# Kernel optimization log

Hardware: AMD Instinct MI355X
Metric: run time of the kernel (lower is better)

## Reference

```python
import itertools
import jax, jax.numpy as jnp
import numpy as np


def _lin(x, w, b):
    # LogitsInference with logic_hidden_dim=[] is a single Linear (logits).
    return jnp.einsum('...i,oi->...o', x, w) + b


def _permute_cat(x, order):
    # Permutation(order): concat over all permutations of the `order` variable axes.
    if order <= 1:
        return x
    nd = x.ndim  # [B, n x order, C]
    return jnp.concatenate(
        [jnp.transpose(x, (0,) + p + (nd - 1,))
         for p in itertools.permutations(range(1, order + 1))], axis=-1)


def _expand(x, i, n):
    # Expander(i-1): insert a new object axis at position i (after existing var axes).
    x = jnp.expand_dims(x, axis=i)
    shape = list(x.shape)
    shape[i] = n
    return jnp.broadcast_to(x, tuple(shape))


def _reduce(x, order_in):
    # Reducer(order_in, exclude_self=True): mask entries with repeated indices among
    # the order_in variable axes, then take exists(max)/forall(min) over the last
    # variable axis and interleave channels -> 2*C.
    n = x.shape[1]
    if order_in >= 2:
        idx = [jnp.arange(n).reshape((1,) * k + (n,) + (1,) * (order_in - k - 1))
               for k in range(order_in)]
        mask = jnp.ones((n,) * order_in, dtype=bool)
        for a in range(order_in):
            for b in range(a + 1, order_in):
                mask = mask & (idx[a] != idx[b])
        mask = mask[None, ..., None]  # [1, n x order_in, 1]
        inp0 = jnp.where(mask, x, jnp.zeros((), x.dtype))
        inp1 = jnp.where(mask, x, jnp.ones((), x.dtype))
    else:
        inp0 = inp1 = x
    exists = jnp.max(inp0, axis=-2)
    forall = jnp.min(inp1, axis=-2)
    out = jnp.stack([exists, forall], axis=-1)  # interleave like torch stack+view
    return out.reshape(out.shape[:-2] + (out.shape[-2] * 2,))


def _bmask(act, bit, ndim):
    return act[:, bit].astype(jnp.float32).reshape((-1,) + (1,) * (ndim - 1))


def _logic_layer(x0, x1, x2, x3,
                 w_op0, b_op0, w_red0, b_red0,
                 w_exp1, b_exp1, w_op1, b_op1, w_red1, b_red1,
                 w_exp2, b_exp2, w_op2, b_op2, w_red2, b_red2,
                 w_exp3, b_exp3, w_op3, b_op3, act):
    n = x1.shape[1]
    # Per-batch-item bit masks replace index_select/index_copy_ (same math:
    # selected rows get the branch output, others contribute zero to the sum).
    # order 0: bits 0 (direct), 1 (reduce from order 1)
    s0 = (_bmask(act, 0, 2) * _lin(x0, w_op0, b_op0)
          + _bmask(act, 1, 2) * _lin(_reduce(x1, 1), w_red0, b_red0))
    o0 = jnp.where(jnp.any(act[:, 0:2] == 1), jax.nn.sigmoid(s0), jnp.zeros_like(s0))
    # order 1: bits 2 (expand from 0), 3 (direct), 4 (reduce from 2)
    s1 = (_bmask(act, 2, 3) * _lin(_expand(x0, 1, n), w_exp1, b_exp1)
          + _bmask(act, 3, 3) * _lin(x1, w_op1, b_op1)
          + _bmask(act, 4, 3) * _lin(_reduce(x2, 2), w_red1, b_red1))
    o1 = jnp.where(jnp.any(act[:, 2:5] == 1), jax.nn.sigmoid(s1), jnp.zeros_like(s1))
    # order 2: bits 5 (expand), 6 (direct), 7 (reduce)
    s2 = (_bmask(act, 5, 4) * _lin(_permute_cat(_expand(x1, 2, n), 2), w_exp2, b_exp2)
          + _bmask(act, 6, 4) * _lin(_permute_cat(x2, 2), w_op2, b_op2)
          + _bmask(act, 7, 4) * _lin(_permute_cat(_reduce(x3, 3), 2), w_red2, b_red2))
    o2 = jnp.where(jnp.any(act[:, 5:8] == 1), jax.nn.sigmoid(s2), jnp.zeros_like(s2))
    # order 3 (= max_order): bits 8 (expand), 9 (direct)
    s3 = (_bmask(act, 8, 5) * _lin(_permute_cat(_expand(x2, 3, n), 3), w_exp3, b_exp3)
          + _bmask(act, 9, 5) * _lin(_permute_cat(x3, 3), w_op3, b_op3))
    o3 = jnp.where(jnp.any(act[:, 8:10] == 1), jax.nn.sigmoid(s3), jnp.zeros_like(s3))
    return (o0, o1, o2, o3)


def setup_inputs() -> dict:
    key = jax.random.key(0)
    B, n, C, O = 8, 32, 64, 64
    ks = list(jax.random.split(key, 32))
    ki = iter(ks)
    d = {}
    d['x0'] = jax.random.normal(next(ki), (B, C), jnp.float32)
    d['x1'] = jax.random.normal(next(ki), (B, n, C), jnp.float32)
    d['x2'] = jax.random.normal(next(ki), (B, n, n, C), jnp.float32)
    d['x3'] = jax.random.normal(next(ki), (B, n, n, n, C), jnp.float32)
    in_dims = {'w_op0': C, 'w_red0': 2 * C,
               'w_exp1': C, 'w_op1': C, 'w_red1': 2 * C,
               'w_exp2': 2 * C, 'w_op2': 2 * C, 'w_red2': 4 * C,
               'w_exp3': 6 * C, 'w_op3': 6 * C}
    for name, ind in in_dims.items():
        d[name] = jax.random.normal(next(ki), (O, ind), jnp.float32) * 0.05
        d['b' + name[1:]] = jnp.zeros((O,), jnp.float32)
    d['act'] = jax.random.randint(next(ki), (B, 10), 0, 2, dtype=jnp.int32)
    return d


def reference(x0, x1, x2, x3,
              w_op0, b_op0, w_red0, b_red0,
              w_exp1, b_exp1, w_op1, b_op1, w_red1, b_red1,
              w_exp2, b_exp2, w_op2, b_op2, w_red2, b_red2,
              w_exp3, b_exp3, w_op3, b_op3, act):
    return _logic_layer(x0, x1, x2, x3,
                        w_op0, b_op0, w_red0, b_red0,
                        w_exp1, b_exp1, w_op1, b_op1, w_red1, b_red1,
                        w_exp2, b_exp2, w_op2, b_op2, w_red2, b_red2,
                        w_exp3, b_exp3, w_op3, b_op3, act)
```

## Files before the change

### kernel.cpp

```cpp
#include <hip/hip_runtime.h>
#include <hip/hip_bf16.h>
#include <math.h>

#define NB 8
#define NN 32
#define NC 64
#define NO 64

#define WS_G    0
#define WS_MF   16
#define WS_R1   128
#define WS_R2   2048
#define WS_X1B  36864
#define WS_X2B  45056
#define WS_R3B  307200
#define WS_BB   831488
#define WS_BB2  832000
#define WS_WC   832512
#define WS_WC2  1029120
#define WS_R2B  1160192
#define WS_WC1  1176576
#define WS_X0B  1242112
#define WS_BB1  1242368

typedef short bf16x8 __attribute__((ext_vector_type(8)));
typedef unsigned short u16x4 __attribute__((ext_vector_type(4)));
typedef float f32x4 __attribute__((ext_vector_type(4)));

__device__ __forceinline__ float sigmoidf_(float s) {
    return 1.0f / (1.0f + expf(-s));
}

__device__ __forceinline__ unsigned short f2b(float x) {
    union { __hip_bfloat16 h; unsigned short u; } v;
    v.h = __float2bfloat16(x);
    return v.u;
}

__device__ __forceinline__ float b2f(unsigned short u) {
    union { unsigned int u; float f; } v; v.u = ((unsigned int)u) << 16;
    return v.f;
}

__global__ __launch_bounds__(256) void prep_all(
        const float* __restrict__ x0, const float* __restrict__ x1,
        const float* __restrict__ x2,
        const float* __restrict__ we3, const float* __restrict__ wo3,
        const float* __restrict__ we2, const float* __restrict__ wo2,
        const float* __restrict__ wr2,
        const float* __restrict__ we1, const float* __restrict__ wo1,
        const float* __restrict__ wr1,
        const float* __restrict__ be1, const float* __restrict__ bo1,
        const float* __restrict__ br1,
        const float* __restrict__ be2, const float* __restrict__ bo2,
        const float* __restrict__ br2,
        const float* __restrict__ be3, const float* __restrict__ bo3,
        const int* __restrict__ act, float* __restrict__ ws) {
    __shared__ float pmx[4][64], pmn[4][64];
    int bb = blockIdx.x, t = threadIdx.x;
    if (bb < 1536) {
        int tid = bb * 256 + t;
        unsigned short* wc = (unsigned short*)(ws + WS_WC);
        int i8 = tid & 7;
        int lane = (tid >> 3) & 63;
        int rest = tid >> 9;
        int kk = rest % 24;
        int ntb = rest / 24;
        int nt = ntb & 3, b = ntb >> 2;
        int o = nt * 16 + (lane & 15);
        int kloc = kk * 32 + ((lane >> 4) << 3) + i8;
        bool m8 = act[b * 10 + 8] == 1;
        bool m9 = act[b * 10 + 9] == 1;
        float val;
        if (kloc < 384) val = m8 ? we3[o * 384 + kloc] : 0.0f;
        else            val = m9 ? wo3[o * 384 + kloc - 384] : 0.0f;
        wc[tid] = f2b(val);
    } else if (bb < 2560) {
        int tid = (bb - 1536) * 256 + t;
        unsigned short* wc2 = (unsigned short*)(ws + WS_WC2);
        int i8 = tid & 7;
        int lane = (tid >> 3) & 63;
        int rest = tid >> 9;
        int kk = rest & 15;
        int ntb = rest >> 4;
        int nt = ntb & 3, b = ntb >> 2;
        int o = nt * 16 + (lane & 15);
        int kloc = kk * 32 + ((lane >> 4) << 3) + i8;
        float val;
        if (kloc < 128)      val = (act[b * 10 + 5] == 1) ? we2[o * 128 + kloc] : 0.0f;
        else if (kloc < 256) val = (act[b * 10 + 6] == 1) ? wo2[o * 128 + kloc - 128] : 0.0f;
        else                 val = (act[b * 10 + 7] == 1) ? wr2[o * 256 + kloc - 256] : 0.0f;
        wc2[tid] = f2b(val);
    } else if (bb < 3072) {
        int tid = (bb - 2560) * 256 + t;
        unsigned short* wc1 = (unsigned short*)(ws + WS_WC1);
        int i8 = tid & 7;
        int lane = (tid >> 3) & 63;
        int rest = tid >> 9;
        int kk = rest & 7;
        int ntb = rest >> 3;
        int nt = ntb & 3, b = ntb >> 2;
        int o = nt * 16 + (lane & 15);
        int kloc = kk * 32 + ((lane >> 4) << 3) + i8;
        float val;
        if (kloc < 64)       val = (act[b * 10 + 2] == 1) ? we1[o * 64 + kloc] : 0.0f;
        else if (kloc < 128) val = (act[b * 10 + 3] == 1) ? wo1[o * 64 + kloc - 64] : 0.0f;
        else                 val = (act[b * 10 + 4] == 1) ? wr1[o * 128 + kloc - 128] : 0.0f;
        wc1[tid] = f2b(val);
    } else if (bb < 3074) {
        int t512 = (bb - 3072) * 256 + t;
        int b = t512 >> 6, o = t512 & 63;
        float m2 = (act[b * 10 + 2] == 1) ? 1.0f : 0.0f;
        float m3 = (act[b * 10 + 3] == 1) ? 1.0f : 0.0f;
        float m4 = (act[b * 10 + 4] == 1) ? 1.0f : 0.0f;
        float m5 = (act[b * 10 + 5] == 1) ? 1.0f : 0.0f;
        float m6 = (act[b * 10 + 6] == 1) ? 1.0f : 0.0f;
        float m7 = (act[b * 10 + 7] == 1) ? 1.0f : 0.0f;
        float m8 = (act[b * 10 + 8] == 1) ? 1.0f : 0.0f;
        float m9 = (act[b * 10 + 9] == 1) ? 1.0f : 0.0f;
        ws[WS_BB1 + t512] = m2 * be1[o] + m3 * bo1[o] + m4 * br1[o];
        ws[WS_BB2 + t512] = m5 * be2[o] + m6 * bo2[o] + m7 * br2[o];
        ws[WS_BB  + t512] = m8 * be3[o] + m9 * bo3[o];
        unsigned short* x0b = (unsigned short*)(ws + WS_X0B);
        x0b[t512] = f2b(x0[t512]);
        if (t512 < 80) ws[WS_MF + t512] = (act[t512] == 1) ? 1.0f : 0.0f;
        if (t512 < 4) {
            const int lo[4] = {0, 2, 5, 8};
            const int hi[4] = {2, 5, 8, 10};
            int any = 0;
            for (int bx = 0; bx < NB; ++bx)
                for (int bit = lo[t512]; bit < hi[t512]; ++bit)
                    any |= (act[bx * 10 + bit] == 1);
            ws[WS_G + t512] = any ? 1.0f : 0.0f;
        }
    } else if (bb < 3082) {
        if (t < 64) {
            int b = bb - 3074, c = t;
            unsigned short* x1b = (unsigned short*)(ws + WS_X1B);
            float mx = -INFINITY, mn = INFINITY;
            for (int k = 0; k < NN; ++k) {
                float v = x1[(b * NN + k) * NC + c];
                x1b[(b * NN + k) * NC + c] = f2b(v);
                mx = fmaxf(mx, v); mn = fminf(mn, v);
            }
            ws[WS_R1 + b * 2 * NC + 2 * c]     = mx;
            ws[WS_R1 + b * 2 * NC + 2 * c + 1] = mn;
        }
    } else {
        int idx = bb - 3082;
        int i = idx & 31, b = idx >> 5;
        int w = t >> 6, c = t & 63;
        unsigned short* x2b = (unsigned short*)(ws + WS_X2B);
        float mx = -INFINITY, mn = INFINITY;
        #pragma unroll
        for (int q = 0; q < 8; ++q) {
            int jj = w * 8 + q;
            float v = x2[((b * NN + i) * NN + jj) * NC + c];
            x2b[((b * NN + i) * NN + jj) * NC + c] = f2b(v);
            mx = fmaxf(mx, (jj == i) ? 0.0f : v);
            mn = fminf(mn, (jj == i) ? 1.0f : v);
        }
        pmx[w][c] = mx; pmn[w][c] = mn;
        __syncthreads();
        if (t < 64) {
            mx = fmaxf(fmaxf(pmx[0][c], pmx[1][c]), fmaxf(pmx[2][c], pmx[3][c]));
            mn = fminf(fminf(pmn[0][c], pmn[1][c]), fminf(pmn[2][c], pmn[3][c]));
            unsigned short* r2b = (unsigned short*)(ws + WS_R2B);
            unsigned int packed = (unsigned int)f2b(mx) | ((unsigned int)f2b(mn) << 16);
            *(unsigned int*)(r2b + (b * NN + i) * 128 + 2 * c) = packed;
        }
    }
}

__global__ __launch_bounds__(256) void out3k_pair(
        const float* __restrict__ x3, const float* __restrict__ ws_f,
        float* __restrict__ out) {
    __shared__ unsigned short A[32 * 768];
    int blk = blockIdx.x;
    int b = blk / 528, pi = blk - b * 528;
    float fsq = sqrtf(4225.0f - 8.0f * (float)pi);
    int i = (int)((65.0f - fsq) * 0.5f);
    while (i > 0 && (i * (65 - i)) / 2 > pi) --i;
    while (((i + 1) * (64 - i)) / 2 <= pi) ++i;
    int j = i + (pi - (i * (65 - i)) / 2);

    int t = threadIdx.x;
    int lane = t & 63, wv = t >> 6;
    const unsigned short* x2b = (const unsigned short*)(ws_f + WS_X2B);
    const unsigned short* wc = (const unsigned short*)(ws_f + WS_WC);
    char* Ab = (char*)A;

    {
        int r8 = t >> 3, c8 = (t & 7) << 3;
        size_t cb[6]; int cs[6];
        cb[0] = ((b * 32 + i) * 32 + j) * 64; cs[0] = 0;
        cb[1] = ((b * 32 + i) * 32) * 64;     cs[1] = 64;
        cb[2] = ((b * 32 + j) * 32 + i) * 64; cs[2] = 0;
        cb[3] = (b * 1024 + i) * 64;          cs[3] = 2048;
        cb[4] = ((b * 32 + j) * 32) * 64;     cs[4] = 64;
        cb[5] = (b * 1024 + j) * 64;          cs[5] = 2048;
        int sw = (r8 & 7) << 4;
        #pragma unroll
        for (int ch = 0; ch < 6; ++ch) {
            bf16x8 v = *(const bf16x8*)(x2b + cb[ch] + (size_t)r8 * cs[ch] + c8);
            *(bf16x8*)(Ab + ((r8 * 1536 + (ch * 64 + c8) * 2) ^ sw)) = v;
        }
        int r16 = t >> 4, c4 = (t & 15) << 2;
        const float* xb[6]; int xs[6];
        xb[0] = x3 + (size_t)(((b * 32 + i) * 32 + j) * 32) * 64; xs[0] = 64;
        xb[1] = x3 + (size_t)(((b * 32 + i) * 32) * 32 + j) * 64; xs[1] = 2048;
        xb[2] = x3 + (size_t)(((b * 32 + j) * 32 + i) * 32) * 64; xs[2] = 64;
        xb[3] = x3 + (size_t)((b * 1024 + i) * 32 + j) * 64;      xs[3] = 65536;
        xb[4] = x3 + (size_t)(((b * 32 + j) * 32) * 32 + i) * 64; xs[4] = 2048;
        xb[5] = x3 + (size_t)(b * 32768 + j * 32 + i) * 64;       xs[5] = 65536;
        #pragma unroll
        for (int ch = 0; ch < 6; ++ch) {
            #pragma unroll
            for (int p = 0; p < 2; ++p) {
                int k = p * 16 + r16;
                f32x4 v = *(const f32x4*)(xb[ch] + (size_t)k * xs[ch] + c4);
                u16x4 hh = { f2b(v[0]), f2b(v[1]), f2b(v[2]), f2b(v[3]) };
                *(u16x4*)(Ab + ((k * 1536 + ((6 + ch) * 64 + c4) * 2) ^ ((k & 7) << 4))) = hh;
            }
        }
    }
    __syncthreads();

    f32x4 acc00 = {0.f,0.f,0.f,0.f}, acc01 = {0.f,0.f,0.f,0.f};
    f32x4 acc10 = {0.f,0.f,0.f,0.f}, acc11 = {0.f,0.f,0.f,0.f};
    const unsigned short* wblk = wc + (size_t)((b * 4 + wv) * 24) * 512 + lane * 8;
    int arow = lane & 15;
    int kgrp2 = ((lane >> 4) << 3) * 2;
    int sw0 = (arow & 7) << 4;
    const int P1[12] = {2, 4, 0, 5, 1, 3, 8, 10, 6, 11, 7, 9};
    #pragma unroll
    for (int c = 0; c < 12; ++c) {
        #pragma unroll
        for (int s = 0; s < 2; ++s) {
            int colb = c * 128 + s * 64 + kgrp2;
            bf16x8 a0 = *(const bf16x8*)(Ab + ((arow * 1536 + colb) ^ sw0));
            bf16x8 a1 = *(const bf16x8*)(Ab + (((arow + 16) * 1536 + colb) ^ sw0));
            bf16x8 w0 = *(const bf16x8*)(wblk + (2 * c + s) * 512);
            bf16x8 w1 = *(const bf16x8*)(wblk + (2 * P1[c] + s) * 512);
            acc00 = __builtin_amdgcn_mfma_f32_16x16x32_bf16(a0, w0, acc00, 0, 0, 0);
            acc01 = __builtin_amdgcn_mfma_f32_16x16x32_bf16(a1, w0, acc01, 0, 0, 0);
            acc10 = __builtin_amdgcn_mfma_f32_16x16x32_bf16(a0, w1, acc10, 0, 0, 0);
            acc11 = __builtin_amdgcn_mfma_f32_16x16x32_bf16(a1, w1, acc11, 0, 0, 0);
        }
    }

    if (wv == 0 || (wv == 1 && i != j)) {
        int c = lane;
        int colbase = (wv == 0) ? 384 : 512;
        float mx = 0.0f, mn = 1.0f;
        if (i != j) {
            for (int k = 0; k < 32; ++k) {
                if (k == i || k == j) continue;
                int addr = (k * 1536 + (colbase + c) * 2) ^ ((k & 7) << 4);
                float v = b2f(*(const unsigned short*)(Ab + addr));
                mx = fmaxf(mx, v); mn = fminf(mn, v);
            }
        }
        unsigned short* r3b = (unsigned short*)(ws_f + WS_R3B);
        int slot = (wv == 0) ? ((b * 32 + i) * 32 + j) : ((b * 32 + j) * 32 + i);
        unsigned int packed = (unsigned int)f2b(mx) | ((unsigned int)f2b(mn) << 16);
        *(unsigned int*)(r3b + (size_t)slot * 128 + 2 * c) = packed;
    }

    float g3 = ws_f[WS_G + 3];
    int o = wv * 16 + (lane & 15);
    float bias = ws_f[WS_BB + b * 64 + o];
    int rgrp = (lane >> 4) << 2;
    float* ob0 = out + (size_t)(((b * 32 + i) * 32 + j) * 32) * 64;
    float* ob1 = out + (size_t)(((b * 32 + j) * 32 + i) * 32) * 64;
    #pragma unroll
    for (int r = 0; r < 4; ++r) {
        float s0 = acc00[r] + bias;
        float s1 = acc01[r] + bias;
        ob0[(rgrp + r) * 64 + o]      = (g3 != 0.0f) ? sigmoidf_(s0) : 0.0f;
        ob0[(16 + rgrp + r) * 64 + o] = (g3 != 0.0f) ? sigmoidf_(s1) : 0.0f;
    }
    if (i != j) {
        #pragma unroll
        for (int r = 0; r < 4; ++r) {
            float s0 = acc10[r] + bias;
            float s1 = acc11[r] + bias;
            ob1[(rgrp + r) * 64 + o]      = (g3 != 0.0f) ? sigmoidf_(s0) : 0.0f;
            ob1[(16 + rgrp + r) * 64 + o] = (g3 != 0.0f) ? sigmoidf_(s1) : 0.0f;
        }
    }
}

__global__ __launch_bounds__(256) void out01(
        const float* __restrict__ x0,
        const float* __restrict__ w_op0, const float* __restrict__ b_op0,
        const float* __restrict__ w_red0, const float* __restrict__ b_red0,
        const float* __restrict__ ws_f, float* __restrict__ out0,
        float* __restrict__ out1) {
    __shared__ unsigned short A[32 * 256];
    int bb = blockIdx.x, t = threadIdx.x;
    if (bb < 8) {
        if (t >= 64) return;
        int b = bb, o = t;
        float g  = ws_f[WS_G + 0];
        float m0 = ws_f[WS_MF + b * 10 + 0], m1 = ws_f[WS_MF + b * 10 + 1];
        float d0 = b_op0[o];
        for (int c = 0; c < NC; ++c) d0 += w_op0[o * NC + c] * x0[b * NC + c];
        float d1 = b_red0[o];
        for (int c = 0; c < 2 * NC; ++c) d1 += w_red0[o * 2 * NC + c] * ws_f[WS_R1 + b * 2 * NC + c];
        float s = m0 * d0 + m1 * d1;
        out0[b * NO + o] = (g != 0.0f) ? sigmoidf_(s) : 0.0f;
        return;
    }
    int b = bb - 8;
    int lane = t & 63, nt = t >> 6;
    const unsigned short* x0b = (const unsigned short*)(ws_f + WS_X0B);
    const unsigned short* x1b = (const unsigned short*)(ws_f + WS_X1B);
    const unsigned short* r2b = (const unsigned short*)(ws_f + WS_R2B);
    const unsigned short* wc1 = (const unsigned short*)(ws_f + WS_WC1);
    char* Ab = (char*)A;
    int r = t >> 3, c8 = (t & 7) << 3;
    int sw = (r & 7) << 4;
    {
        bf16x8 v0 = *(const bf16x8*)(x0b + b * 64 + c8);
        bf16x8 v1 = *(const bf16x8*)(x1b + (b * 32 + r) * 64 + c8);
        bf16x8 v2 = *(const bf16x8*)(r2b + (b * 32 + r) * 128 + c8);
        bf16x8 v3 = *(const bf16x8*)(r2b + (b * 32 + r) * 128 + 64 + c8);
        *(bf16x8*)(Ab + ((r * 512 + (0 * 64 + c8) * 2) ^ sw)) = v0;
        *(bf16x8*)(Ab + ((r * 512 + (1 * 64 + c8) * 2) ^ sw)) = v1;
        *(bf16x8*)(Ab + ((r * 512 + (2 * 64 + c8) * 2) ^ sw)) = v2;
        *(bf16x8*)(Ab + ((r * 512 + (3 * 64 + c8) * 2) ^ sw)) = v3;
    }
    __syncthreads();
    f32x4 acc0 = {0.f,0.f,0.f,0.f};
    f32x4 acc1 = {0.f,0.f,0.f,0.f};
    const unsigned short* wblk = wc1 + (size_t)((b * 4 + nt) * 8) * 512 + lane * 8;
    int arow0 = lane & 15, arow1 = 16 + arow0;
    int kgrp2 = ((lane >> 4) << 3) * 2;
    int sw0 = (arow0 & 7) << 4;
    #pragma unroll
    for (int kk = 0; kk < 8; ++kk) {
        int kloc2 = kk * 64 + kgrp2;
        bf16x8 a0 = *(const bf16x8*)(Ab + ((arow0 * 512 + kloc2) ^ sw0));
        bf16x8 a1 = *(const bf16x8*)(Ab + ((arow1 * 512 + kloc2) ^ sw0));
        bf16x8 bw = *(const bf16x8*)(wblk + kk * 512);
        acc0 = __builtin_amdgcn_mfma_f32_16x16x32_bf16(a0, bw, acc0, 0, 0, 0);
        acc1 = __builtin_amdgcn_mfma_f32_16x16x32_bf16(a1, bw, acc1, 0, 0, 0);
    }
    float g1 = ws_f[WS_G + 1];
    int o = nt * 16 + (lane & 15);
    float bias = ws_f[WS_BB1 + b * 64 + o];
    int rgrp = (lane >> 4) << 2;
    float* obase = out1 + b * 2048;
    #pragma unroll
    for (int rr = 0; rr < 4; ++rr) {
        float s0 = acc0[rr] + bias;
        float s1 = acc1[rr] + bias;
        obase[(rgrp + rr) * 64 + o]      = (g1 != 0.0f) ? sigmoidf_(s0) : 0.0f;
        obase[(16 + rgrp + rr) * 64 + o] = (g1 != 0.0f) ? sigmoidf_(s1) : 0.0f;
    }
}

__global__ __launch_bounds__(256) void out2k_mfma(
        const float* __restrict__ ws_f, float* __restrict__ out) {
    __shared__ unsigned short A[32 * 512];
    int blk = blockIdx.x;
    int i = blk & 31, b = blk >> 5;
    int t = threadIdx.x;
    int lane = t & 63, nt = t >> 6;
    const unsigned short* x1b = (const unsigned short*)(ws_f + WS_X1B);
    const unsigned short* x2b = (const unsigned short*)(ws_f + WS_X2B);
    const unsigned short* r3b = (const unsigned short*)(ws_f + WS_R3B);
    const unsigned short* wc2 = (const unsigned short*)(ws_f + WS_WC2);
    char* Ab = (char*)A;
    int r8 = t >> 3, c8 = (t & 7) << 3;
    {
        bf16x8 v0 = *(const bf16x8*)(x1b + (b * 32 + i) * 64 + c8);
        bf16x8 v1 = *(const bf16x8*)(x1b + b * 2048 + r8 * 64 + c8);
        bf16x8 v2 = *(const bf16x8*)(x2b + ((b * 32 + i) * 32) * 64 + r8 * 64 + c8);
        bf16x8 v3 = *(const bf16x8*)(x2b + (b * 1024 + i) * 64 + r8 * 2048 + c8);
        int sw = (r8 & 7) << 4;
        *(bf16x8*)(Ab + ((r8 * 1024 + (0 * 64 + c8) * 2) ^ sw)) = v0;
        *(bf16x8*)(Ab + ((r8 * 1024 + (1 * 64 + c8) * 2) ^ sw)) = v1;
        *(bf16x8*)(Ab + ((r8 * 1024 + (2 * 64 + c8) * 2) ^ sw)) = v2;
        *(bf16x8*)(Ab + ((r8 * 1024 + (3 * 64 + c8) * 2) ^ sw)) = v3;
    }
    int r16 = t >> 4, c16 = (t & 15) << 3;
    #pragma unroll
    for (int p = 0; p < 2; ++p) {
        int jr = p * 16 + r16;
        bf16x8 v4 = *(const bf16x8*)(r3b + ((b * 32 + i) * 32 + jr) * 128 + c16);
        bf16x8 v5 = *(const bf16x8*)(r3b + ((b * 32 + jr) * 32 + i) * 128 + c16);
        int sw = (jr & 7) << 4;
        *(bf16x8*)(Ab + ((jr * 1024 + (256 + c16) * 2) ^ sw)) = v4;
        *(bf16x8*)(Ab + ((jr * 1024 + (384 + c16) * 2) ^ sw)) = v5;
    }
    __syncthreads();
    f32x4 acc0 = {0.f,0.f,0.f,0.f};
    f32x4 acc1 = {0.f,0.f,0.f,0.f};
    const unsigned short* wblk = wc2 + (size_t)((b * 4 + nt) * 16) * 512 + lane * 8;
    int arow0 = lane & 15, arow1 = 16 + arow0;
    int kgrp2 = ((lane >> 4) << 3) * 2;
    int sw0 = (arow0 & 7) << 4;
    #pragma unroll
    for (int kk = 0; kk < 16; ++kk) {
        int kloc2 = kk * 64 + kgrp2;
        bf16x8 a0 = *(const bf16x8*)(Ab + ((arow0 * 1024 + kloc2) ^ sw0));
        bf16x8 a1 = *(const bf16x8*)(Ab + ((arow1 * 1024 + kloc2) ^ sw0));
        bf16x8 bf = *(const bf16x8*)(wblk + kk * 512);
        acc0 = __builtin_amdgcn_mfma_f32_16x16x32_bf16(a0, bf, acc0, 0, 0, 0);
        acc1 = __builtin_amdgcn_mfma_f32_16x16x32_bf16(a1, bf, acc1, 0, 0, 0);
    }
    float g2 = ws_f[WS_G + 2];
    int o = nt * 16 + (lane & 15);
    float bias = ws_f[WS_BB2 + b * 64 + o];
    int rgrp = (lane >> 4) << 2;
    float* obase = out + (size_t)((b * 32 + i) * 32) * 64;
    #pragma unroll
    for (int r = 0; r < 4; ++r) {
        float s0 = acc0[r] + bias;
        float s1 = acc1[r] + bias;
        obase[(rgrp + r) * 64 + o]      = (g2 != 0.0f) ? sigmoidf_(s0) : 0.0f;
        obase[(16 + rgrp + r) * 64 + o] = (g2 != 0.0f) ? sigmoidf_(s1) : 0.0f;
    }
}

extern "C" void kernel_launch(void* const* d_in, const int* in_sizes, int n_in,
                              void* d_out, int out_size, void* d_ws, size_t ws_size,
                              hipStream_t stream) {
    const float* x0 = (const float*)d_in[0];
    const float* x1 = (const float*)d_in[1];
    const float* x2 = (const float*)d_in[2];
    const float* x3 = (const float*)d_in[3];
    const float* w_op0 = (const float*)d_in[4];   const float* b_op0 = (const float*)d_in[5];
    const float* w_red0 = (const float*)d_in[6];  const float* b_red0 = (const float*)d_in[7];
    const float* w_exp1 = (const float*)d_in[8];  const float* b_exp1 = (const float*)d_in[9];
    const float* w_op1 = (const float*)d_in[10];  const float* b_op1 = (const float*)d_in[11];
    const float* w_red1 = (const float*)d_in[12]; const float* b_red1 = (const float*)d_in[13];
    const float* w_exp2 = (const float*)d_in[14]; const float* b_exp2 = (const float*)d_in[15];
    const float* w_op2 = (const float*)d_in[16];  const float* b_op2 = (const float*)d_in[17];
    const float* w_red2 = (const float*)d_in[18]; const float* b_red2 = (const float*)d_in[19];
    const float* w_exp3 = (const float*)d_in[20]; const float* b_exp3 = (const float*)d_in[21];
    const float* w_op3 = (const float*)d_in[22];  const float* b_op3 = (const float*)d_in[23];
    const int* act = (const int*)d_in[24];

    float* ws = (float*)d_ws;
    float* out = (float*)d_out;
    float* out0 = out;
    float* out1 = out + 512;
    float* out2 = out + 16896;
    float* out3 = out + 541184;

    prep_all<<<3338, 256, 0, stream>>>(x0, x1, x2,
                                       w_exp3, w_op3, w_exp2, w_op2, w_red2,
                                       w_exp1, w_op1, w_red1,
                                       b_exp1, b_op1, b_red1,
                                       b_exp2, b_op2, b_red2,
                                       b_exp3, b_op3, act, ws);
    out3k_pair<<<NB * 528, 256, 0, stream>>>(x3, ws, out3);
    out01<<<16, 256, 0, stream>>>(x0, w_op0, b_op0, w_red0, b_red0, ws, out0, out1);
    out2k_mfma<<<NB * NN, 256, 0, stream>>>(ws, out2);
}
```

Before: 228.4 us.

## Double out3k_pair block to 512 threads splitting M rows across waves

Raises the out3k_pair block to 8 waves: each wave now computes one 16-row half of the 32-row tile per output column group, holding two accumulators instead of four. Staging loads are redistributed so each thread loads half as many x2/x3 rows. Block index mapping is changed so the batch index is the fastest-varying dimension, spreading consecutive blocks across batches. The aim is more latency hiding and shorter per-wave staging and MFMA chains. The cost is duplicated weight-fragment loads across the two M halves and possibly lower occupancy, since the 48KB shared tile per block is unchanged.

```diff
diff --git a/kernel.cpp b/kernel.cpp
--- a/kernel.cpp
+++ b/kernel.cpp
@@ -10,7 +10,6 @@
 #define WS_G    0
 #define WS_MF   16
 #define WS_R1   128
-#define WS_R2   2048
 #define WS_X1B  36864
 #define WS_X2B  45056
 #define WS_R3B  307200
@@ -172,12 +171,12 @@
     }
 }
 
-__global__ __launch_bounds__(256) void out3k_pair(
+__global__ __launch_bounds__(512) void out3k_pair(
         const float* __restrict__ x3, const float* __restrict__ ws_f,
         float* __restrict__ out) {
     __shared__ unsigned short A[32 * 768];
     int blk = blockIdx.x;
-    int b = blk / 528, pi = blk - b * 528;
+    int b = blk & 7, pi = blk >> 3;
     float fsq = sqrtf(4225.0f - 8.0f * (float)pi);
     int i = (int)((65.0f - fsq) * 0.5f);
     while (i > 0 && (i * (65 - i)) / 2 > pi) --i;
@@ -186,12 +185,14 @@
 
     int t = threadIdx.x;
     int lane = t & 63, wv = t >> 6;
+    int nt = wv & 3, mh = wv >> 2;
     const unsigned short* x2b = (const unsigned short*)(ws_f + WS_X2B);
     const unsigned short* wc = (const unsigned short*)(ws_f + WS_WC);
     char* Ab = (char*)A;
 
     {
-        int r8 = t >> 3, c8 = (t & 7) << 3;
+        int r8 = (t >> 3) & 31, c8 = (t & 7) << 3;
+        int cset = (t >> 8) * 3;
         size_t cb[6]; int cs[6];
         cb[0] = ((b * 32 + i) * 32 + j) * 64; cs[0] = 0;
         cb[1] = ((b * 32 + i) * 32) * 64;     cs[1] = 64;
@@ -201,11 +202,12 @@
         cb[5] = (b * 1024 + j) * 64;          cs[5] = 2048;
         int sw = (r8 & 7) << 4;
         #pragma unroll
-        for (int ch = 0; ch < 6; ++ch) {
+        for (int cc = 0; cc < 3; ++cc) {
+            int ch = cset + cc;
             bf16x8 v = *(const bf16x8*)(x2b + cb[ch] + (size_t)r8 * cs[ch] + c8);
             *(bf16x8*)(Ab + ((r8 * 1536 + (ch * 64 + c8) * 2) ^ sw)) = v;
         }
-        int r16 = t >> 4, c4 = (t & 15) << 2;
+        int r32 = t >> 4, c4 = (t & 15) << 2;
         const float* xb[6]; int xs[6];
         xb[0] = x3 + (size_t)(((b * 32 + i) * 32 + j) * 32) * 64; xs[0] = 64;
         xb[1] = x3 + (size_t)(((b * 32 + i) * 32) * 32 + j) * 64; xs[1] = 2048;
@@ -213,43 +215,37 @@
         xb[3] = x3 + (size_t)((b * 1024 + i) * 32 + j) * 64;      xs[3] = 65536;
         xb[4] = x3 + (size_t)(((b * 32 + j) * 32) * 32 + i) * 64; xs[4] = 2048;
         xb[5] = x3 + (size_t)(b * 32768 + j * 32 + i) * 64;       xs[5] = 65536;
+        int sw2 = (r32 & 7) << 4;
         #pragma unroll
         for (int ch = 0; ch < 6; ++ch) {
-            #pragma unroll
-            for (int p = 0; p < 2; ++p) {
-                int k = p * 16 + r16;
-                f32x4 v = *(const f32x4*)(xb[ch] + (size_t)k * xs[ch] + c4);
-                u16x4 hh = { f2b(v[0]), f2b(v[1]), f2b(v[2]), f2b(v[3]) };
-                *(u16x4*)(Ab + ((k * 1536 + ((6 + ch) * 64 + c4) * 2) ^ ((k & 7) << 4))) = hh;
-            }
+            f32x4 v = *(const f32x4*)(xb[ch] + (size_t)r32 * xs[ch] + c4);
+            u16x4 hh = { f2b(v[0]), f2b(v[1]), f2b(v[2]), f2b(v[3]) };
+            *(u16x4*)(Ab + ((r32 * 1536 + ((6 + ch) * 64 + c4) * 2) ^ sw2)) = hh;
         }
     }
     __syncthreads();
 
-    f32x4 acc00 = {0.f,0.f,0.f,0.f}, acc01 = {0.f,0.f,0.f,0.f};
-    f32x4 acc10 = {0.f,0.f,0.f,0.f}, acc11 = {0.f,0.f,0.f,0.f};
-    const unsigned short* wblk = wc + (size_t)((b * 4 + wv) * 24) * 512 + lane * 8;
-    int arow = lane & 15;
+    f32x4 accI = {0.f,0.f,0.f,0.f};
+    f32x4 accJ = {0.f,0.f,0.f,0.f};
+    const unsigned short* wblk = wc + (size_t)((b * 4 + nt) * 24) * 512 + lane * 8;
+    int arow = (lane & 15) + mh * 16;
     int kgrp2 = ((lane >> 4) << 3) * 2;
-    int sw0 = (arow & 7) << 4;
+    int sw0 = ((lane & 15) & 7) << 4;
     const int P1[12] = {2, 4, 0, 5, 1, 3, 8, 10, 6, 11, 7, 9};
     #pragma unroll
     for (int c = 0; c < 12; ++c) {
         #pragma unroll
         for (int s = 0; s < 2; ++s) {
             int colb = c * 128 + s * 64 + kgrp2;
-            bf16x8 a0 = *(const bf16x8*)(Ab + ((arow * 1536 + colb) ^ sw0));
-            bf16x8 a1 = *(const bf16x8*)(Ab + (((arow + 16) * 1536 + colb) ^ sw0));
+            bf16x8 a = *(const bf16x8*)(Ab + ((arow * 1536 + colb) ^ sw0));
             bf16x8 w0 = *(const bf16x8*)(wblk + (2 * c + s) * 512);
             bf16x8 w1 = *(const bf16x8*)(wblk + (2 * P1[c] + s) * 512);
-            acc00 = __builtin_amdgcn_mfma_f32_16x16x32_bf16(a0, w0, acc00, 0, 0, 0);
-            acc01 = __builtin_amdgcn_mfma_f32_16x16x32_bf16(a1, w0, acc01, 0, 0, 0);
-            acc10 = __builtin_amdgcn_mfma_f32_16x16x32_bf16(a0, w1, acc10, 0, 0, 0);
-            acc11 = __builtin_amdgcn_mfma_f32_16x16x32_bf16(a1, w1, acc11, 0, 0, 0);
-        }
-    }
-
-    if (wv == 0 || (wv == 1 && i != j)) {
+            accI = __builtin_amdgcn_mfma_f32_16x16x32_bf16(a, w0, accI, 0, 0, 0);
+            accJ = __builtin_amdgcn_mfma_f32_16x16x32_bf16(a, w1, accJ, 0, 0, 0);
+        }
+    }
+
+    if (wv == 0 || (wv == 4 && i != j)) {
         int c = lane;
         int colbase = (wv == 0) ? 384 : 512;
         float mx = 0.0f, mn = 1.0f;
@@ -268,25 +264,21 @@
     }
 
     float g3 = ws_f[WS_G + 3];
-    int o = wv * 16 + (lane & 15);
+    int o = nt * 16 + (lane & 15);
     float bias = ws_f[WS_BB + b * 64 + o];
-    int rgrp = (lane >> 4) << 2;
+    int row0 = mh * 16 + ((lane >> 4) << 2);
     float* ob0 = out + (size_t)(((b * 32 + i) * 32 + j) * 32) * 64;
     float* ob1 = out + (size_t)(((b * 32 + j) * 32 + i) * 32) * 64;
     #pragma unroll
     for (int r = 0; r < 4; ++r) {
-        float s0 = acc00[r] + bias;
-        float s1 = acc01[r] + bias;
-        ob0[(rgrp + r) * 64 + o]      = (g3 != 0.0f) ? sigmoidf_(s0) : 0.0f;
-        ob0[(16 + rgrp + r) * 64 + o] = (g3 != 0.0f) ? sigmoidf_(s1) : 0.0f;
+        float s0 = accI[r] + bias;
+        ob0[(row0 + r) * 64 + o] = (g3 != 0.0f) ? sigmoidf_(s0) : 0.0f;
     }
     if (i != j) {
         #pragma unroll
         for (int r = 0; r < 4; ++r) {
-            float s0 = acc10[r] + bias;
-            float s1 = acc11[r] + bias;
-            ob1[(rgrp + r) * 64 + o]      = (g3 != 0.0f) ? sigmoidf_(s0) : 0.0f;
-            ob1[(16 + rgrp + r) * 64 + o] = (g3 != 0.0f) ? sigmoidf_(s1) : 0.0f;
+            float s1 = accJ[r] + bias;
+            ob1[(row0 + r) * 64 + o] = (g3 != 0.0f) ? sigmoidf_(s1) : 0.0f;
         }
     }
 }
@@ -457,7 +449,7 @@
                                        b_exp1, b_op1, b_red1,
                                        b_exp2, b_op2, b_red2,
                                        b_exp3, b_op3, act, ws);
-    out3k_pair<<<NB * 528, 256, 0, stream>>>(x3, ws, out3);
+    out3k_pair<<<NB * 528, 512, 0, stream>>>(x3, ws, out3);
     out01<<<16, 256, 0, stream>>>(x0, w_op0, b_op0, w_red0, b_red0, ws, out0, out1);
     out2k_mfma<<<NB * NN, 256, 0, stream>>>(ws, out2);
 }
```

After: 229.4 us. No clear change (+0.5%).
